# Performance work log

Measured on AMD Instinct MI355X. Metric: run time of the kernel, lower is better.

Reference implementation:

```python
import jax, jax.numpy as jnp
import numpy as np

CODEBOOK_SIZE = 1024
EMBED_DIM = 64
COMMITMENT_COST = 0.25


def setup_inputs() -> dict:
    key = jax.random.key(0)
    k1, k2 = jax.random.split(key)
    z = jax.random.normal(k1, (8, EMBED_DIM, 8192), dtype=jnp.float32)
    # torch init: uniform(-1/codebook_size, 1/codebook_size)
    codebook_weight = jax.random.uniform(
        k2, (CODEBOOK_SIZE, EMBED_DIM), dtype=jnp.float32,
        minval=-1.0 / CODEBOOK_SIZE, maxval=1.0 / CODEBOOK_SIZE)
    return {"z": z, "codebook_weight": codebook_weight}


def reference(z, codebook_weight):
    B, D, T = z.shape
    # [B*T, D]
    z_flat = jnp.transpose(z, (0, 2, 1)).reshape(-1, D)
    # squared euclidean distances to each code: ||z||^2 - 2 z.W^T + ||W||^2
    distances = (jnp.sum(z_flat * z_flat, axis=1, keepdims=True)
                 - 2.0 * z_flat @ codebook_weight.T
                 + jnp.sum(codebook_weight * codebook_weight, axis=1))
    codes = jnp.argmin(distances, axis=1)  # [B*T]
    z_q = codebook_weight[codes].reshape(B, T, D).transpose(0, 2, 1)  # [B, D, T]
    commitment_loss = jnp.mean((jax.lax.stop_gradient(z_q) - z) ** 2)
    codebook_loss = jnp.mean((z_q - jax.lax.stop_gradient(z)) ** 2)
    vq_loss = codebook_loss + COMMITMENT_COST * commitment_loss
    # straight-through estimator
    z_q_st = z + jax.lax.stop_gradient(z_q - z)
    return z_q_st, vq_loss, codes
```

## Files before the change

kernel.cpp:

```cpp
#include <hip/hip_runtime.h>


#define T_DIM 8192
#define D_DIM 64
#define C_DIM 1024
#define B_DIM 8
#define NROWS (B_DIM * T_DIM)
#define NELEM (B_DIM * D_DIM * T_DIM)
#define SEGS 2
#define EPI_BLOCKS (NELEM / 4 / 256)

#define R64(M) M(0) M(1) M(2) M(3) M(4) M(5) M(6) M(7) \
  M(8) M(9) M(10) M(11) M(12) M(13) M(14) M(15) \
  M(16) M(17) M(18) M(19) M(20) M(21) M(22) M(23) \
  M(24) M(25) M(26) M(27) M(28) M(29) M(30) M(31) \
  M(32) M(33) M(34) M(35) M(36) M(37) M(38) M(39) \
  M(40) M(41) M(42) M(43) M(44) M(45) M(46) M(47) \
  M(48) M(49) M(50) M(51) M(52) M(53) M(54) M(55) \
  M(56) M(57) M(58) M(59) M(60) M(61) M(62) M(63)

#define SQ_(x) __fmul_rn(x, x)
#define AD_(a, b) __fadd_rn(a, b)

#define PAIRWISE64(p, dst) \
  float pr0 = SQ_(p##0);  pr0 = AD_(pr0, SQ_(p##8));  pr0 = AD_(pr0, SQ_(p##16)); pr0 = AD_(pr0, SQ_(p##24)); pr0 = AD_(pr0, SQ_(p##32)); pr0 = AD_(pr0, SQ_(p##40)); pr0 = AD_(pr0, SQ_(p##48)); pr0 = AD_(pr0, SQ_(p##56)); \
  float pr1 = SQ_(p##1);  pr1 = AD_(pr1, SQ_(p##9));  pr1 = AD_(pr1, SQ_(p##17)); pr1 = AD_(pr1, SQ_(p##25)); pr1 = AD_(pr1, SQ_(p##33)); pr1 = AD_(pr1, SQ_(p##41)); pr1 = AD_(pr1, SQ_(p##49)); pr1 = AD_(pr1, SQ_(p##57)); \
  float pr2 = SQ_(p##2);  pr2 = AD_(pr2, SQ_(p##10)); pr2 = AD_(pr2, SQ_(p##18)); pr2 = AD_(pr2, SQ_(p##26)); pr2 = AD_(pr2, SQ_(p##34)); pr2 = AD_(pr2, SQ_(p##42)); pr2 = AD_(pr2, SQ_(p##50)); pr2 = AD_(pr2, SQ_(p##58)); \
  float pr3 = SQ_(p##3);  pr3 = AD_(pr3, SQ_(p##11)); pr3 = AD_(pr3, SQ_(p##19)); pr3 = AD_(pr3, SQ_(p##27)); pr3 = AD_(pr3, SQ_(p##35)); pr3 = AD_(pr3, SQ_(p##43)); pr3 = AD_(pr3, SQ_(p##51)); pr3 = AD_(pr3, SQ_(p##59)); \
  float pr4 = SQ_(p##4);  pr4 = AD_(pr4, SQ_(p##12)); pr4 = AD_(pr4, SQ_(p##20)); pr4 = AD_(pr4, SQ_(p##28)); pr4 = AD_(pr4, SQ_(p##36)); pr4 = AD_(pr4, SQ_(p##44)); pr4 = AD_(pr4, SQ_(p##52)); pr4 = AD_(pr4, SQ_(p##60)); \
  float pr5 = SQ_(p##5);  pr5 = AD_(pr5, SQ_(p##13)); pr5 = AD_(pr5, SQ_(p##21)); pr5 = AD_(pr5, SQ_(p##29)); pr5 = AD_(pr5, SQ_(p##37)); pr5 = AD_(pr5, SQ_(p##45)); pr5 = AD_(pr5, SQ_(p##53)); pr5 = AD_(pr5, SQ_(p##61)); \
  float pr6 = SQ_(p##6);  pr6 = AD_(pr6, SQ_(p##14)); pr6 = AD_(pr6, SQ_(p##22)); pr6 = AD_(pr6, SQ_(p##30)); pr6 = AD_(pr6, SQ_(p##38)); pr6 = AD_(pr6, SQ_(p##46)); pr6 = AD_(pr6, SQ_(p##54)); pr6 = AD_(pr6, SQ_(p##62)); \
  float pr7 = SQ_(p##7);  pr7 = AD_(pr7, SQ_(p##15)); pr7 = AD_(pr7, SQ_(p##23)); pr7 = AD_(pr7, SQ_(p##31)); pr7 = AD_(pr7, SQ_(p##39)); pr7 = AD_(pr7, SQ_(p##47)); pr7 = AD_(pr7, SQ_(p##55)); pr7 = AD_(pr7, SQ_(p##63)); \
  float dst = AD_(AD_(AD_(pr0, pr1), AD_(pr2, pr3)), AD_(AD_(pr4, pr5), AD_(pr6, pr7)));

#define WSQ_OF(arr, dst) float dst; { \
  float c0 = SQ_(arr[0].x); c0=AD_(c0,SQ_(arr[2].x)); c0=AD_(c0,SQ_(arr[4].x)); c0=AD_(c0,SQ_(arr[6].x)); c0=AD_(c0,SQ_(arr[8].x)); c0=AD_(c0,SQ_(arr[10].x)); c0=AD_(c0,SQ_(arr[12].x)); c0=AD_(c0,SQ_(arr[14].x)); \
  float c1 = SQ_(arr[0].y); c1=AD_(c1,SQ_(arr[2].y)); c1=AD_(c1,SQ_(arr[4].y)); c1=AD_(c1,SQ_(arr[6].y)); c1=AD_(c1,SQ_(arr[8].y)); c1=AD_(c1,SQ_(arr[10].y)); c1=AD_(c1,SQ_(arr[12].y)); c1=AD_(c1,SQ_(arr[14].y)); \
  float c2 = SQ_(arr[0].z); c2=AD_(c2,SQ_(arr[2].z)); c2=AD_(c2,SQ_(arr[4].z)); c2=AD_(c2,SQ_(arr[6].z)); c2=AD_(c2,SQ_(arr[8].z)); c2=AD_(c2,SQ_(arr[10].z)); c2=AD_(c2,SQ_(arr[12].z)); c2=AD_(c2,SQ_(arr[14].z)); \
  float c3 = SQ_(arr[0].w); c3=AD_(c3,SQ_(arr[2].w)); c3=AD_(c3,SQ_(arr[4].w)); c3=AD_(c3,SQ_(arr[6].w)); c3=AD_(c3,SQ_(arr[8].w)); c3=AD_(c3,SQ_(arr[10].w)); c3=AD_(c3,SQ_(arr[12].w)); c3=AD_(c3,SQ_(arr[14].w)); \
  float c4 = SQ_(arr[1].x); c4=AD_(c4,SQ_(arr[3].x)); c4=AD_(c4,SQ_(arr[5].x)); c4=AD_(c4,SQ_(arr[7].x)); c4=AD_(c4,SQ_(arr[9].x)); c4=AD_(c4,SQ_(arr[11].x)); c4=AD_(c4,SQ_(arr[13].x)); c4=AD_(c4,SQ_(arr[15].x)); \
  float c5 = SQ_(arr[1].y); c5=AD_(c5,SQ_(arr[3].y)); c5=AD_(c5,SQ_(arr[5].y)); c5=AD_(c5,SQ_(arr[7].y)); c5=AD_(c5,SQ_(arr[9].y)); c5=AD_(c5,SQ_(arr[11].y)); c5=AD_(c5,SQ_(arr[13].y)); c5=AD_(c5,SQ_(arr[15].y)); \
  float c6 = SQ_(arr[1].z); c6=AD_(c6,SQ_(arr[3].z)); c6=AD_(c6,SQ_(arr[5].z)); c6=AD_(c6,SQ_(arr[7].z)); c6=AD_(c6,SQ_(arr[9].z)); c6=AD_(c6,SQ_(arr[11].z)); c6=AD_(c6,SQ_(arr[13].z)); c6=AD_(c6,SQ_(arr[15].z)); \
  float c7 = SQ_(arr[1].w); c7=AD_(c7,SQ_(arr[3].w)); c7=AD_(c7,SQ_(arr[5].w)); c7=AD_(c7,SQ_(arr[7].w)); c7=AD_(c7,SQ_(arr[9].w)); c7=AD_(c7,SQ_(arr[11].w)); c7=AD_(c7,SQ_(arr[13].w)); c7=AD_(c7,SQ_(arr[15].w)); \
  dst = AD_(AD_(AD_(c0, c1), AD_(c2, c3)), AD_(AD_(c4, c5), AD_(c6, c7))); }

__global__ __launch_bounds__(256, 2)
void vq_dist_kernel(const float* __restrict__ z,
                    const float* __restrict__ cb,
                    float2* __restrict__ pairs) {
    const int tid  = threadIdx.x;
    const int wid  = tid >> 6;
    const int lane = tid & 63;
    const int seg  = blockIdx.y;
    const int row0 = blockIdx.x * 256;
    const int b    = row0 >> 13;
    const int t0   = row0 & (T_DIM - 1);

    __shared__ float4 zl[16][256];
    __shared__ float  zsql[256];
    __shared__ float2 res[4][256];

    {
        const float* zp = z + (size_t)b * (D_DIM * T_DIM) + (t0 + tid);
#define LOADZ(k) float z##k = zp[(size_t)k * T_DIM];
        R64(LOADZ)
#undef LOADZ
        PAIRWISE64(z, zsq)
        zsql[tid] = zsq;
        zl[ 0][tid] = make_float4(z0,  z1,  z2,  z3);
        zl[ 1][tid] = make_float4(z4,  z5,  z6,  z7);
        zl[ 2][tid] = make_float4(z8,  z9,  z10, z11);
        zl[ 3][tid] = make_float4(z12, z13, z14, z15);
        zl[ 4][tid] = make_float4(z16, z17, z18, z19);
        zl[ 5][tid] = make_float4(z20, z21, z22, z23);
        zl[ 6][tid] = make_float4(z24, z25, z26, z27);
        zl[ 7][tid] = make_float4(z28, z29, z30, z31);
        zl[ 8][tid] = make_float4(z32, z33, z34, z35);
        zl[ 9][tid] = make_float4(z36, z37, z38, z39);
        zl[10][tid] = make_float4(z40, z41, z42, z43);
        zl[11][tid] = make_float4(z44, z45, z46, z47);
        zl[12][tid] = make_float4(z48, z49, z50, z51);
        zl[13][tid] = make_float4(z52, z53, z54, z55);
        zl[14][tid] = make_float4(z56, z57, z58, z59);
        zl[15][tid] = make_float4(z60, z61, z62, z63);
    }

    const int cbase = seg * 512 + wid * 128;
    const int cA = cbase + lane;
    const int cB = cA + 64;
    float4 wa[16], wb[16];
    {
        const float4* wpa = (const float4*)(cb + ((size_t)cA << 6));
        const float4* wpb = (const float4*)(cb + ((size_t)cB << 6));
#pragma unroll
        for (int kk = 0; kk < 16; ++kk) { wa[kk] = wpa[kk]; wb[kk] = wpb[kk]; }
    }
    WSQ_OF(wa, wsqA)
    WSQ_OF(wb, wsqB)
    __syncthreads();

#pragma unroll 1
    for (int r = 0; r < 256; r += 4) {
        float aA0 = 0.f, aA1 = 0.f, aA2 = 0.f, aA3 = 0.f;
        float aB0 = 0.f, aB1 = 0.f, aB2 = 0.f, aB3 = 0.f;
#pragma unroll
        for (int kk = 0; kk < 16; ++kk) {
            const float4 zc0 = zl[kk][r + 0];
            const float4 zc1 = zl[kk][r + 1];
            const float4 zc2 = zl[kk][r + 2];
            const float4 zc3 = zl[kk][r + 3];
            const float4 WA = wa[kk];
            const float4 WB = wb[kk];
            aA0 = fmaf(zc0.x, WA.x, aA0); aA0 = fmaf(zc0.y, WA.y, aA0);
            aA0 = fmaf(zc0.z, WA.z, aA0); aA0 = fmaf(zc0.w, WA.w, aA0);
            aB0 = fmaf(zc0.x, WB.x, aB0); aB0 = fmaf(zc0.y, WB.y, aB0);
            aB0 = fmaf(zc0.z, WB.z, aB0); aB0 = fmaf(zc0.w, WB.w, aB0);
            aA1 = fmaf(zc1.x, WA.x, aA1); aA1 = fmaf(zc1.y, WA.y, aA1);
            aA1 = fmaf(zc1.z, WA.z, aA1); aA1 = fmaf(zc1.w, WA.w, aA1);
            aB1 = fmaf(zc1.x, WB.x, aB1); aB1 = fmaf(zc1.y, WB.y, aB1);
            aB1 = fmaf(zc1.z, WB.z, aB1); aB1 = fmaf(zc1.w, WB.w, aB1);
            aA2 = fmaf(zc2.x, WA.x, aA2); aA2 = fmaf(zc2.y, WA.y, aA2);
            aA2 = fmaf(zc2.z, WA.z, aA2); aA2 = fmaf(zc2.w, WA.w, aA2);
            aB2 = fmaf(zc2.x, WB.x, aB2); aB2 = fmaf(zc2.y, WB.y, aB2);
            aB2 = fmaf(zc2.z, WB.z, aB2); aB2 = fmaf(zc2.w, WB.w, aB2);
            aA3 = fmaf(zc3.x, WA.x, aA3); aA3 = fmaf(zc3.y, WA.y, aA3);
            aA3 = fmaf(zc3.z, WA.z, aA3); aA3 = fmaf(zc3.w, WA.w, aA3);
            aB3 = fmaf(zc3.x, WB.x, aB3); aB3 = fmaf(zc3.y, WB.y, aB3);
            aB3 = fmaf(zc3.z, WB.z, aB3); aB3 = fmaf(zc3.w, WB.w, aB3);
        }
        const float zr0 = zsql[r + 0];
        const float zr1 = zsql[r + 1];
        const float zr2 = zsql[r + 2];
        const float zr3 = zsql[r + 3];
        const float dA0 = __fadd_rn(__fsub_rn(zr0, __fmul_rn(2.0f, aA0)), wsqA);
        const float dB0 = __fadd_rn(__fsub_rn(zr0, __fmul_rn(2.0f, aB0)), wsqB);
        const float dA1 = __fadd_rn(__fsub_rn(zr1, __fmul_rn(2.0f, aA1)), wsqA);
        const float dB1 = __fadd_rn(__fsub_rn(zr1, __fmul_rn(2.0f, aB1)), wsqB);
        const float dA2 = __fadd_rn(__fsub_rn(zr2, __fmul_rn(2.0f, aA2)), wsqA);
        const float dB2 = __fadd_rn(__fsub_rn(zr2, __fmul_rn(2.0f, aB2)), wsqB);
        const float dA3 = __fadd_rn(__fsub_rn(zr3, __fmul_rn(2.0f, aA3)), wsqA);
        const float dB3 = __fadd_rn(__fsub_rn(zr3, __fmul_rn(2.0f, aB3)), wsqB);
        const bool tB0 = (dB0 < dA0); const float d0 = tB0 ? dB0 : dA0;
        const bool tB1 = (dB1 < dA1); const float d1 = tB1 ? dB1 : dA1;
        const bool tB2 = (dB2 < dA2); const float d2 = tB2 ? dB2 : dA2;
        const bool tB3 = (dB3 < dA3); const float d3 = tB3 ? dB3 : dA3;
        float m0 = d0, m1 = d1, m2 = d2, m3 = d3;
#pragma unroll
        for (int off = 32; off > 0; off >>= 1) {
            m0 = fminf(m0, __shfl_xor(m0, off, 64));
            m1 = fminf(m1, __shfl_xor(m1, off, 64));
            m2 = fminf(m2, __shfl_xor(m2, off, 64));
            m3 = fminf(m3, __shfl_xor(m3, off, 64));
        }
#define ARGMIN_J(mj, dj, tBj, outIdx) { \
        const unsigned long long mskA = __ballot((!tBj) && (dj == mj)); \
        const unsigned long long mskB = __ballot(tBj && (dj == mj)); \
        int code; \
        if (mskA) code = cbase + (__ffsll((long long)mskA) - 1); \
        else      code = cbase + 64 + (__ffsll((long long)mskB) - 1); \
        if (lane == 0) res[wid][outIdx] = make_float2(mj, (float)code); }
        ARGMIN_J(m0, d0, tB0, r + 0)
        ARGMIN_J(m1, d1, tB1, r + 1)
        ARGMIN_J(m2, d2, tB2, r + 2)
        ARGMIN_J(m3, d3, tB3, r + 3)
#undef ARGMIN_J
    }
    __syncthreads();

    {
        float2 best = res[0][tid];
#pragma unroll
        for (int w = 1; w < 4; ++w) {
            const float2 p = res[w][tid];
            if (p.x < best.x) best = p;
        }
        pairs[seg * NROWS + row0 + tid] = best;
    }
}

__global__ void vq_argmin_kernel(const float2* __restrict__ pairs,
                                 float* __restrict__ codes) {
    int row = blockIdx.x * blockDim.x + threadIdx.x;
    float2 best = pairs[row];
#pragma unroll
    for (int s = 1; s < SEGS; ++s) {
        float2 p = pairs[s * NROWS + row];
        if (p.x < best.x) best = p;
    }
    codes[row] = best.y;
}

__global__ void vq_epilogue_kernel(const float* __restrict__ z,
                                   const float* __restrict__ cb,
                                   const float* __restrict__ codes,
                                   float* __restrict__ out,
                                   double* __restrict__ partials) {
    const int q = blockIdx.x * 256 + threadIdx.x;
    const int i = q << 2;
    const int t = i & (T_DIM - 1);
    const int bd = i >> 13;
    const int d = bd & (D_DIM - 1);
    const int b = bd >> 6;
    const int row = (b << 13) | t;

    float4 cr = *(const float4*)(codes + row);
    float4 zv = *(const float4*)(z + i);
    float w0 = cb[((int)cr.x << 6) + d];
    float w1 = cb[((int)cr.y << 6) + d];
    float w2 = cb[((int)cr.z << 6) + d];
    float w3 = cb[((int)cr.w << 6) + d];

    float4 df = make_float4(w0 - zv.x, w1 - zv.y, w2 - zv.z, w3 - zv.w);
    float4 o = make_float4(zv.x + df.x, zv.y + df.y, zv.z + df.z, zv.w + df.w);
    *(float4*)(out + i) = o;

    double v = (double)df.x * df.x + (double)df.y * df.y +
               (double)df.z * df.z + (double)df.w * df.w;
#pragma unroll
    for (int o2 = 32; o2 > 0; o2 >>= 1) v += __shfl_down(v, o2, 64);

    __shared__ double red[4];
    if ((threadIdx.x & 63) == 0) red[threadIdx.x >> 6] = v;
    __syncthreads();
    if (threadIdx.x == 0)
        partials[blockIdx.x] = ((red[0] + red[1]) + (red[2] + red[3]));
}

__global__ void vq_loss_kernel(const double* __restrict__ partials,
                               float* __restrict__ out_loss) {
    double s = 0.0;
    for (int i = threadIdx.x; i < EPI_BLOCKS; i += 256) s += partials[i];
#pragma unroll
    for (int o = 32; o > 0; o >>= 1) s += __shfl_down(s, o, 64);
    __shared__ double red[4];
    if ((threadIdx.x & 63) == 0) red[threadIdx.x >> 6] = s;
    __syncthreads();
    if (threadIdx.x == 0) {
        double tot = (red[0] + red[1]) + (red[2] + red[3]);
        out_loss[0] = (float)(1.25 * tot / (double)NELEM);
    }
}

extern "C" void kernel_launch(void* const* d_in, const int* in_sizes, int n_in,
                              void* d_out, int out_size, void* d_ws, size_t ws_size,
                              hipStream_t stream) {
    const float* z  = (const float*)d_in[0];
    const float* cb = (const float*)d_in[1];

    float* out      = (float*)d_out;
    float* out_loss = out + NELEM;
    float* codes    = out + NELEM + 1;

    char* ws    = (char*)d_ws;
    double* partials = (double*)(ws);
    float2* pairs = (float2*)(ws + 32768);

    dim3 grid1(NROWS / 256, SEGS);
    vq_dist_kernel<<<grid1, 256, 0, stream>>>(z, cb, pairs);

    vq_argmin_kernel<<<NROWS / 256, 256, 0, stream>>>(pairs, codes);

    vq_epilogue_kernel<<<EPI_BLOCKS, 256, 0, stream>>>(z, cb, codes, out, partials);

    vq_loss_kernel<<<1, 256, 0, stream>>>(partials, out_loss);
}
```

Before: 241.1 us.

## Fuse distance, argmin and epilogue into one 512-thread kernel per row tile

Merges the distance kernel, the cross-segment argmin kernel and the epilogue into one kernel. Each 512-thread block now covers all 1024 codes for 256 rows instead of splitting codes across two blocks. The epilogue reuses the z tile already held in shared memory and the codes just computed, which removes the pairs round-trip and the second read of z. In exchange the grid halves to 256 blocks, which may reduce occupancy across CUs, and the epilogue's codebook gathers and strided stores are done with scalar accesses.

```diff
diff --git a/kernel.cpp b/kernel.cpp
--- a/kernel.cpp
+++ b/kernel.cpp
@@ -7,8 +7,7 @@
 #define B_DIM 8
 #define NROWS (B_DIM * T_DIM)
 #define NELEM (B_DIM * D_DIM * T_DIM)
-#define SEGS 2
-#define EPI_BLOCKS (NELEM / 4 / 256)
+#define NBLKS (NROWS / 256)
 
 #define R64(M) M(0) M(1) M(2) M(3) M(4) M(5) M(6) M(7) \
   M(8) M(9) M(10) M(11) M(12) M(13) M(14) M(15) \
@@ -44,23 +43,25 @@
   float c7 = SQ_(arr[1].w); c7=AD_(c7,SQ_(arr[3].w)); c7=AD_(c7,SQ_(arr[5].w)); c7=AD_(c7,SQ_(arr[7].w)); c7=AD_(c7,SQ_(arr[9].w)); c7=AD_(c7,SQ_(arr[11].w)); c7=AD_(c7,SQ_(arr[13].w)); c7=AD_(c7,SQ_(arr[15].w)); \
   dst = AD_(AD_(AD_(c0, c1), AD_(c2, c3)), AD_(AD_(c4, c5), AD_(c6, c7))); }
 
-__global__ __launch_bounds__(256, 2)
-void vq_dist_kernel(const float* __restrict__ z,
-                    const float* __restrict__ cb,
-                    float2* __restrict__ pairs) {
+__global__ __launch_bounds__(512, 2)
+void vq_fused_kernel(const float* __restrict__ z,
+                     const float* __restrict__ cb,
+                     float* __restrict__ out,
+                     float* __restrict__ codes,
+                     double* __restrict__ partials) {
     const int tid  = threadIdx.x;
     const int wid  = tid >> 6;
     const int lane = tid & 63;
-    const int seg  = blockIdx.y;
     const int row0 = blockIdx.x * 256;
     const int b    = row0 >> 13;
     const int t0   = row0 & (T_DIM - 1);
 
     __shared__ float4 zl[16][256];
     __shared__ float  zsql[256];
-    __shared__ float2 res[4][256];
-
-    {
+    __shared__ float2 res[8][256];
+    __shared__ int    codesl[256];
+
+    if (tid < 256) {
         const float* zp = z + (size_t)b * (D_DIM * T_DIM) + (t0 + tid);
 #define LOADZ(k) float z##k = zp[(size_t)k * T_DIM];
         R64(LOADZ)
@@ -85,7 +86,7 @@
         zl[15][tid] = make_float4(z60, z61, z62, z63);
     }
 
-    const int cbase = seg * 512 + wid * 128;
+    const int cbase = wid * 128;
     const int cA = cbase + lane;
     const int cB = cA + 64;
     float4 wa[16], wb[16];
@@ -167,69 +168,50 @@
     }
     __syncthreads();
 
-    {
+    if (tid < 256) {
         float2 best = res[0][tid];
 #pragma unroll
-        for (int w = 1; w < 4; ++w) {
+        for (int w = 1; w < 8; ++w) {
             const float2 p = res[w][tid];
             if (p.x < best.x) best = p;
         }
-        pairs[seg * NROWS + row0 + tid] = best;
-    }
-}
-
-__global__ void vq_argmin_kernel(const float2* __restrict__ pairs,
-                                 float* __restrict__ codes) {
-    int row = blockIdx.x * blockDim.x + threadIdx.x;
-    float2 best = pairs[row];
-#pragma unroll
-    for (int s = 1; s < SEGS; ++s) {
-        float2 p = pairs[s * NROWS + row];
-        if (p.x < best.x) best = p;
-    }
-    codes[row] = best.y;
-}
-
-__global__ void vq_epilogue_kernel(const float* __restrict__ z,
-                                   const float* __restrict__ cb,
-                                   const float* __restrict__ codes,
-                                   float* __restrict__ out,
-                                   double* __restrict__ partials) {
-    const int q = blockIdx.x * 256 + threadIdx.x;
-    const int i = q << 2;
-    const int t = i & (T_DIM - 1);
-    const int bd = i >> 13;
-    const int d = bd & (D_DIM - 1);
-    const int b = bd >> 6;
-    const int row = (b << 13) | t;
-
-    float4 cr = *(const float4*)(codes + row);
-    float4 zv = *(const float4*)(z + i);
-    float w0 = cb[((int)cr.x << 6) + d];
-    float w1 = cb[((int)cr.y << 6) + d];
-    float w2 = cb[((int)cr.z << 6) + d];
-    float w3 = cb[((int)cr.w << 6) + d];
-
-    float4 df = make_float4(w0 - zv.x, w1 - zv.y, w2 - zv.z, w3 - zv.w);
-    float4 o = make_float4(zv.x + df.x, zv.y + df.y, zv.z + df.z, zv.w + df.w);
-    *(float4*)(out + i) = o;
-
-    double v = (double)df.x * df.x + (double)df.y * df.y +
-               (double)df.z * df.z + (double)df.w * df.w;
-#pragma unroll
-    for (int o2 = 32; o2 > 0; o2 >>= 1) v += __shfl_down(v, o2, 64);
-
-    __shared__ double red[4];
-    if ((threadIdx.x & 63) == 0) red[threadIdx.x >> 6] = v;
-    __syncthreads();
-    if (threadIdx.x == 0)
-        partials[blockIdx.x] = ((red[0] + red[1]) + (red[2] + red[3]));
+        codes[row0 + tid] = best.y;
+        codesl[tid] = (int)best.y;
+    }
+    __syncthreads();
+
+    const int hi = tid >> 8;
+    const int tl = tid & 255;
+    double lsum = 0.0;
+    float* outb = out + (size_t)b * (D_DIM * T_DIM);
+#pragma unroll 1
+    for (int it = 0; it < 32; ++it) {
+        const int d = (it << 1) + hi;
+        const int code = codesl[tl];
+        const float4 zq4 = zl[d >> 2][tl];
+        const float zv = (d & 3) == 0 ? zq4.x : (d & 3) == 1 ? zq4.y
+                       : (d & 3) == 2 ? zq4.z : zq4.w;
+        const float wv = cb[(code << 6) + d];
+        const float df = __fsub_rn(wv, zv);
+        outb[(size_t)d * T_DIM + (t0 + tl)] = __fadd_rn(zv, df);
+        lsum += (double)df * (double)df;
+    }
+#pragma unroll
+    for (int o2 = 32; o2 > 0; o2 >>= 1) lsum += __shfl_down(lsum, o2, 64);
+    __shared__ double redd[8];
+    if (lane == 0) redd[wid] = lsum;
+    __syncthreads();
+    if (tid == 0) {
+        double t4 = ((redd[0] + redd[1]) + (redd[2] + redd[3]))
+                  + ((redd[4] + redd[5]) + (redd[6] + redd[7]));
+        partials[blockIdx.x] = t4;
+    }
 }
 
 __global__ void vq_loss_kernel(const double* __restrict__ partials,
                                float* __restrict__ out_loss) {
     double s = 0.0;
-    for (int i = threadIdx.x; i < EPI_BLOCKS; i += 256) s += partials[i];
+    for (int i = threadIdx.x; i < NBLKS; i += 256) s += partials[i];
 #pragma unroll
     for (int o = 32; o > 0; o >>= 1) s += __shfl_down(s, o, 64);
     __shared__ double red[4];
@@ -251,16 +233,8 @@
     float* out_loss = out + NELEM;
     float* codes    = out + NELEM + 1;
 
-    char* ws    = (char*)d_ws;
-    double* partials = (double*)(ws);
-    float2* pairs = (float2*)(ws + 32768);
-
-    dim3 grid1(NROWS / 256, SEGS);
-    vq_dist_kernel<<<grid1, 256, 0, stream>>>(z, cb, pairs);
-
-    vq_argmin_kernel<<<NROWS / 256, 256, 0, stream>>>(pairs, codes);
-
-    vq_epilogue_kernel<<<EPI_BLOCKS, 256, 0, stream>>>(z, cb, codes, out, partials);
-
+    double* partials = (double*)d_ws;
+
+    vq_fused_kernel<<<NBLKS, 512, 0, stream>>>(z, cb, out, codes, partials);
     vq_loss_kernel<<<1, 256, 0, stream>>>(partials, out_loss);
 }
```

New measurement: 223.8 us. 7.2% less time.
